# Kernel tuning notes

Hardware: AMD Instinct MI355X
Metric: run time of the kernel (lower is better)

The kernel has to match this reference:

```python
import jax, jax.numpy as jnp
import numpy as np

D_WIN = 6
SIGMA = D_WIN / 2.0  # sigma = D/2
EPS = 1e-6


def _ln(x, g, b):
    m = jnp.mean(x, -1, keepdims=True)
    v = jnp.var(x, -1, keepdims=True)
    return (x - m) / jnp.sqrt(v + EPS) * g + b


def _cross_attn(q, kv, Wq, Wkv, Wproj, bproj, nh):
    # standard multi-head cross attention, no qkv bias (qkv_bias=False)
    B, S, C = q.shape
    N = kv.shape[1]
    hd = C // nh
    scale = hd ** -0.5
    qh = (q @ Wq).reshape(B, S, nh, hd).transpose(0, 2, 1, 3) * scale
    kvh = (kv @ Wkv).reshape(B, N, 2, nh, hd).transpose(2, 0, 3, 1, 4)
    k, v = kvh[0], kvh[1]
    attn = jax.nn.softmax(jnp.einsum('bhsd,bhnd->bhsn', qh, k), -1)
    x = jnp.einsum('bhsn,bhnd->bhsd', attn, v).transpose(0, 2, 1, 3).reshape(B, S, C)
    return x @ Wproj + bproj


def setup_inputs() -> dict:
    key = jax.random.key(0)
    ks = jax.random.split(key, 32)
    B, S, C, H, W = 32, 128, 384, 8, 512

    def lin(k, i, o):
        return jax.random.normal(k, (i, o), jnp.float32) * 0.02

    inp = {
        'q': jax.random.normal(ks[0], (B, S, C), jnp.float32),
        'kv': jax.random.normal(ks[1], (B, H * W, C), jnp.float32),
        # main attention linears (qkv_bias=False)
        'Wq': lin(ks[2], C, C),
        'Wkv': lin(ks[3], C, 2 * C),
        'Wproj': lin(ks[4], C, C), 'bproj': jnp.zeros((C,), jnp.float32),
        # position predictor
        'Wp_w': lin(ks[5], C, C), 'Wp_b': jnp.zeros((C,), jnp.float32),
        'vp_w': lin(ks[6], C, 1), 'vp_b': jnp.zeros((1,), jnp.float32),
        'Wqpos': lin(ks[7], C, C), 'bqpos': jnp.zeros((C,), jnp.float32),
        # simplified RCTC decoder projection
        'Wrctc': lin(ks[8], C, C), 'brctc': jnp.zeros((C,), jnp.float32),
        # pt_to_question cross attention (2 heads)
        'ca1_Wq': lin(ks[9], C, C), 'ca1_Wkv': lin(ks[10], C, 2 * C),
        'ca1_Wproj': lin(ks[11], C, C), 'ca1_bproj': jnp.zeros((C,), jnp.float32),
        # pt_to_image cross attention (2 heads)
        'ca2_Wq': lin(ks[12], C, C), 'ca2_Wkv': lin(ks[13], C, 2 * C),
        'ca2_Wproj': lin(ks[14], C, C), 'ca2_bproj': jnp.zeros((C,), jnp.float32),
        # layernorms
        'g_q1': jnp.ones((C,), jnp.float32), 'b_q1': jnp.zeros((C,), jnp.float32),
        'g_kv1': jnp.ones((C,), jnp.float32), 'b_kv1': jnp.zeros((C,), jnp.float32),
        'g_q2': jnp.ones((C,), jnp.float32), 'b_q2': jnp.zeros((C,), jnp.float32),
        'g_kv2': jnp.ones((C,), jnp.float32), 'b_kv2': jnp.zeros((C,), jnp.float32),
        'sz_h': H, 'sz_w': W,
    }
    return inp


def reference(q, kv, Wq, Wkv, Wproj, bproj, Wp_w, Wp_b, vp_w, vp_b, Wqpos, bqpos,
              Wrctc, brctc, ca1_Wq, ca1_Wkv, ca1_Wproj, ca1_bproj,
              ca2_Wq, ca2_Wkv, ca2_Wproj, ca2_bproj,
              g_q1, b_q1, g_kv1, b_kv1, g_q2, b_q2, g_kv2, b_kv2, sz_h, sz_w):
    B, N, C = kv.shape
    S = q.shape[1]
    H, W = sz_h, sz_w
    nh = 1
    hd = C // nh
    scale = hd ** -0.5

    # RCTC decoder (simplified): (B,N,C) -> (B,C,H,W) -> collapse H -> (B,W,C) -> linear
    kv_img = kv.transpose(0, 2, 1).reshape(B, C, H, W)
    dec = kv_img.mean(axis=2).transpose(0, 2, 1)  # (B, W, C)
    dec = dec @ Wrctc + brctc

    qh = (q @ Wq).reshape(B, S, nh, hd).transpose(0, 2, 1, 3) * scale  # (B,nh,S,hd)
    kvh = (dec @ Wkv).reshape(B, W, 2, nh, hd).transpose(2, 0, 3, 1, 4)
    k, v = kvh[0], kvh[1]  # (B,nh,W,hd)

    # position prediction branch
    p = q @ Wqpos + bqpos
    p = _cross_attn(_ln(p, g_q1, b_q1), _ln(q, g_kv1, b_kv1),
                    ca1_Wq, ca1_Wkv, ca1_Wproj, ca1_bproj, 2)
    p = _cross_attn(_ln(p, g_q2, b_q2), _ln(dec, g_kv2, b_kv2),
                    ca2_Wq, ca2_Wkv, ca2_Wproj, ca2_bproj, 2)
    p_t = jax.nn.sigmoid(jnp.tanh(p @ Wp_w + Wp_b) @ vp_w + vp_b) * W  # (B,S,1)

    # Gaussian window mask around predicted position
    idx = jnp.arange(W, dtype=jnp.float32)[None, None, None, :]     # (1,1,1,W)
    pexp = p_t[:, None, :, :]                                        # (B,1,S,1)
    gauss = jnp.exp(-(idx - pexp) ** 2 / (2.0 * SIGMA ** 2))         # (B,1,S,W)

    attn = jnp.einsum('bhsd,bhwd->bhsw', qh, k) * gauss
    attn = jax.nn.softmax(attn, -1)
    x = jnp.einsum('bhsw,bhwd->bhsd', attn, v).transpose(0, 2, 1, 3).reshape(B, S, C)
    return x @ Wproj + bproj
```

## Files before the change

kernel.cpp:

```cpp
#include <hip/hip_runtime.h>
#include <hip/hip_bf16.h>
#include <math.h>

#define B_ 32
#define S_ 128
#define C_ 384
#define H_ 8
#define W_ 512
#define NKV 4096

typedef __attribute__((ext_vector_type(8))) short short8;
typedef __attribute__((ext_vector_type(4))) float floatx4;

static __device__ __forceinline__ ushort f2bf(float v) {
    __hip_bfloat16 h = __float2bfloat16(v);
    return *(ushort*)&h;
}
static __device__ __forceinline__ float ldf(const float* p, size_t i) { return p[i]; }
static __device__ __forceinline__ float ldf(const ushort* p, size_t i) {
    union { uint u; float f; } c; c.u = (uint)p[i] << 16; return c.f;
}

static __device__ __forceinline__ void gl_lds16(const ushort* g, ushort* l) {
    __builtin_amdgcn_global_load_lds(
        (const __attribute__((address_space(1))) void*)g,
        (__attribute__((address_space(3))) void*)l, 16, 0, 0);
}

__global__ __launch_bounds__(256) void mean_kernel(const float* __restrict__ kv,
                                                   ushort* __restrict__ dec0b) {
    int v = blockIdx.x * blockDim.x + threadIdx.x;
    int total = B_ * W_ * (C_ / 4);
    if (v >= total) return;
    int c4  = v % (C_ / 4);
    int row = v / (C_ / 4);
    int b = row / W_;
    int w = row % W_;
    const float4* src = (const float4*)kv + (size_t)(b * NKV + w) * (C_ / 4) + c4;
    float4 s = {0.f, 0.f, 0.f, 0.f};
#pragma unroll
    for (int h = 0; h < H_; ++h) {
        float4 t = src[(size_t)h * W_ * (C_ / 4)];
        s.x += t.x; s.y += t.y; s.z += t.z; s.w += t.w;
    }
    ushort4 o;
    o.x = f2bf(s.x * 0.125f); o.y = f2bf(s.y * 0.125f);
    o.z = f2bf(s.z * 0.125f); o.w = f2bf(s.w * 0.125f);
    ((ushort4*)dec0b)[v] = o;
}

__global__ __launch_bounds__(256) void cast_kernel(const float* __restrict__ in,
                                                   ushort* __restrict__ out, int n4) {
    int v = blockIdx.x * blockDim.x + threadIdx.x;
    if (v >= n4) return;
    float4 f = ((const float4*)in)[v];
    ushort4 o;
    o.x = f2bf(f.x); o.y = f2bf(f.y); o.z = f2bf(f.z); o.w = f2bf(f.w);
    ((ushort4*)out)[v] = o;
}

struct WtDesc { const float* src[12]; ushort* dst[12]; int Kd[12]; int Nd[12]; };
__global__ __launch_bounds__(256) void wtcast_kernel(WtDesc d) {
    int wi = blockIdx.y;
    int idx = blockIdx.x * 256 + threadIdx.x;
    int K = d.Kd[wi], N = d.Nd[wi];
    if (idx >= K * N) return;
    int n = idx / K, k = idx % K;
    d.dst[wi][idx] = f2bf(d.src[wi][(size_t)k * N + n]);
}

__global__ __launch_bounds__(256) void bgemm_kernel(
    const ushort* __restrict__ A, const ushort* __restrict__ Bt,
    const float* __restrict__ bias, float* __restrict__ Cout,
    ushort* __restrict__ Cbf, int M, int N, int K, float alpha, int act)
{
    __shared__ ushort As[128 * 32];
    __shared__ ushort Bs[128 * 32];
    const int tid = threadIdx.x;
    const int bm = blockIdx.y * 128, bn = blockIdx.x * 128;
    const int wav = tid >> 6, lane = tid & 63;
    const int wm = (wav >> 1) * 64, wn = (wav & 1) * 64;
    const int lrow = lane & 15, lq = lane >> 4;

    floatx4 acc[4][4] = {};

    const int crow = tid >> 2, ccol = (tid & 3) * 8;
    const ushort* Ag0 = A + (size_t)(bm + crow) * K + ccol;
    const ushort* Ag1 = Ag0 + (size_t)64 * K;
    const ushort* Bg0 = Bt + (size_t)(bn + crow) * K + ccol;
    const ushort* Bg1 = Bg0 + (size_t)64 * K;
    ushort* AsP0 = &As[tid * 8];
    ushort* AsP1 = &As[2048 + tid * 8];
    ushort* BsP0 = &Bs[tid * 8];
    ushort* BsP1 = &Bs[2048 + tid * 8];

    for (int k0 = 0; k0 < K; k0 += 32) {
        gl_lds16(Ag0 + k0, AsP0);
        gl_lds16(Ag1 + k0, AsP1);
        gl_lds16(Bg0 + k0, BsP0);
        gl_lds16(Bg1 + k0, BsP1);
        __syncthreads();
        short8 af[4], bfr[4];
#pragma unroll
        for (int i = 0; i < 4; ++i)
            af[i] = *(const short8*)&As[(wm + 16 * i + lrow) * 32 + lq * 8];
#pragma unroll
        for (int j = 0; j < 4; ++j)
            bfr[j] = *(const short8*)&Bs[(wn + 16 * j + lrow) * 32 + lq * 8];
#pragma unroll
        for (int i = 0; i < 4; ++i)
#pragma unroll
            for (int j = 0; j < 4; ++j)
                acc[i][j] = __builtin_amdgcn_mfma_f32_16x16x32_bf16(af[i], bfr[j], acc[i][j], 0, 0, 0);
        __syncthreads();
    }

#pragma unroll
    for (int i = 0; i < 4; ++i)
#pragma unroll
        for (int j = 0; j < 4; ++j) {
            int row = bm + wm + 16 * i + lq * 4;
            int col = bn + wn + 16 * j + lrow;
            float bv = bias ? bias[col] : 0.f;
#pragma unroll
            for (int r = 0; r < 4; ++r) {
                float v = acc[i][j][r] * alpha + bv;
                if (act == 1) v = tanhf(v);
                size_t off = (size_t)(row + r) * N + col;
                if (Cout) Cout[off] = v;
                if (Cbf) Cbf[off] = f2bf(v);
            }
        }
}

static inline void bgemm(hipStream_t st, const ushort* A, const ushort* Bt,
                         const float* bias, float* Cout, ushort* Cbf,
                         int M, int N, int K, float alpha, int act) {
    dim3 grid(N / 128, M / 128), block(256);
    bgemm_kernel<<<grid, block, 0, st>>>(A, Bt, bias, Cout, Cbf, M, N, K, alpha, act);
}

struct BGArgs {
    const ushort* A; const ushort* Bt;
    const float* bias; float* outF; ushort* outB;
    int lda, ldb, ldo;
    long AsB, BsB, OsB;
    int AsH, BsH, OsH;
    int K, NH;
    float alpha; int act;
};
__global__ __launch_bounds__(256) void battn_kernel(BGArgs g) {
    __shared__ ushort As[128 * 40];
    __shared__ ushort Bs[64 * 40];
    const int bn = blockIdx.x * 64, bm = blockIdx.y * 128;
    const int bat = blockIdx.z, bb = bat / g.NH, hh = bat % g.NH;
    const ushort* A  = g.A  + (size_t)bb * g.AsB + (size_t)hh * g.AsH;
    const ushort* Bt = g.Bt + (size_t)bb * g.BsB + (size_t)hh * g.BsH;
    const int tid = threadIdx.x;
    const int wav = tid >> 6, lane = tid & 63;
    const int lrow = lane & 15, lq = lane >> 4;
    const int sr = tid >> 2, sc0 = (tid & 3) * 8;
    const ushort* Ag0 = A + (size_t)(bm + sr) * g.lda + sc0;
    const ushort* Ag1 = A + (size_t)(bm + sr + 64) * g.lda + sc0;
    const ushort* Bg  = Bt + (size_t)(bn + sr) * g.ldb + sc0;
    ushort* Asw0 = &As[sr * 40 + sc0];
    ushort* Asw1 = &As[(sr + 64) * 40 + sc0];
    ushort* Bsw  = &Bs[sr * 40 + sc0];

    floatx4 acc[2][4] = {};

    for (int k0 = 0; k0 < g.K; k0 += 32) {
        uint4 a0 = *(const uint4*)(Ag0 + k0);
        uint4 a1 = *(const uint4*)(Ag1 + k0);
        uint4 b  = *(const uint4*)(Bg + k0);
        __syncthreads();
        *(uint4*)Asw0 = a0; *(uint4*)Asw1 = a1; *(uint4*)Bsw = b;
        __syncthreads();
        short8 af0 = *(const short8*)&As[(wav * 32 + lrow) * 40 + lq * 8];
        short8 af1 = *(const short8*)&As[(wav * 32 + 16 + lrow) * 40 + lq * 8];
#pragma unroll
        for (int j = 0; j < 4; ++j) {
            short8 bf = *(const short8*)&Bs[(16 * j + lrow) * 40 + lq * 8];
            acc[0][j] = __builtin_amdgcn_mfma_f32_16x16x32_bf16(af0, bf, acc[0][j], 0, 0, 0);
            acc[1][j] = __builtin_amdgcn_mfma_f32_16x16x32_bf16(af1, bf, acc[1][j], 0, 0, 0);
        }
    }

#pragma unroll
    for (int i = 0; i < 2; ++i)
#pragma unroll
        for (int j = 0; j < 4; ++j) {
            int col = bn + 16 * j + lrow;
            float bv = g.bias ? g.bias[col] : 0.f;
            int row0 = bm + wav * 32 + 16 * i + lq * 4;
#pragma unroll
            for (int r = 0; r < 4; ++r) {
                float v = acc[i][j][r] * g.alpha + bv;
                if (g.act == 1) v = tanhf(v);
                size_t off = (size_t)bb * g.OsB + (size_t)hh * g.OsH
                           + (size_t)(row0 + r) * g.ldo + col;
                if (g.outF) g.outF[off] = v;
                if (g.outB) g.outB[off] = f2bf(v);
            }
        }
}

static inline void battn(hipStream_t st, const ushort* A, const ushort* Bt,
                         const float* bias, float* outF, ushort* outB,
                         int M, int N, int K, float alpha, int act,
                         int lda, long AsB, int AsH,
                         int ldb, long BsB, int BsH,
                         int ldo, long OsB, int OsH,
                         int NH, int nbat) {
    BGArgs g;
    g.A = A; g.Bt = Bt; g.bias = bias; g.outF = outF; g.outB = outB;
    g.lda = lda; g.ldb = ldb; g.ldo = ldo;
    g.AsB = AsB; g.BsB = BsB; g.OsB = OsB;
    g.AsH = AsH; g.BsH = BsH; g.OsH = OsH;
    g.K = K; g.NH = NH; g.alpha = alpha; g.act = act;
    dim3 grid(N / 64, M / 128, nbat);
    battn_kernel<<<grid, 256, 0, st>>>(g);
}

static inline void bgemm64(hipStream_t st, const ushort* A, const ushort* Bt,
                           const float* bias, float* outF, ushort* outB,
                           int M, int N, int K, float alpha, int act) {
    battn(st, A, Bt, bias, outF, outB, M, N, K, alpha, act,
          K, 0, 0, K, 0, 0, N, 0, 0, 1, 1);
}

template <typename T>
__global__ __launch_bounds__(128) void ln_kernel(const T* __restrict__ X,
    const float* __restrict__ g, const float* __restrict__ bb,
    ushort* __restrict__ Y) {
    int row = blockIdx.x;
    const T* x = X + (size_t)row * C_;
    ushort* y = Y + (size_t)row * C_;
    int t = threadIdx.x;
    float v0 = ldf(x, t), v1 = ldf(x, t + 128), v2 = ldf(x, t + 256);
    float s = v0 + v1 + v2, sq = v0 * v0 + v1 * v1 + v2 * v2;
    __shared__ float rs[128], rq[128];
    rs[t] = s; rq[t] = sq; __syncthreads();
    if (t < 64) {
        s = rs[t] + rs[t + 64]; sq = rq[t] + rq[t + 64];
        for (int o = 32; o; o >>= 1) { s += __shfl_down(s, o); sq += __shfl_down(sq, o); }
        if (t == 0) { rs[0] = s; rq[0] = sq; }
    }
    __syncthreads();
    float mean = rs[0] * (1.0f / C_);
    float var  = rq[0] * (1.0f / C_) - mean * mean;
    float inv  = rsqrtf(var + 1e-6f);
    y[t]       = f2bf((v0 - mean) * inv * g[t]       + bb[t]);
    y[t + 128] = f2bf((v1 - mean) * inv * g[t + 128] + bb[t + 128]);
    y[t + 256] = f2bf((v2 - mean) * inv * g[t + 256] + bb[t + 256]);
}

template <int NW, int GAUSS>
__global__ __launch_bounds__(256) void softmax_kernel(
    const float* __restrict__ sc, const float* __restrict__ ptv,
    ushort* __restrict__ P)
{
    int row = blockIdx.x * 4 + (threadIdx.x >> 6);
    int lane = threadIdx.x & 63;
    const float* s = sc + (size_t)row * NW;
    float pcen = GAUSS ? ptv[row] : 0.f;
    float vals[NW / 64];
    float m = -1e30f;
#pragma unroll
    for (int i = 0; i < NW / 64; ++i) {
        int w = lane + 64 * i;
        float v = s[w];
        if (GAUSS) { float dw = (float)w - pcen; v *= expf(dw * dw * (-1.0f / 18.0f)); }
        vals[i] = v; m = fmaxf(m, v);
    }
#pragma unroll
    for (int o = 32; o; o >>= 1) m = fmaxf(m, __shfl_xor(m, o));
    float sum = 0.f;
#pragma unroll
    for (int i = 0; i < NW / 64; ++i) { vals[i] = expf(vals[i] - m); sum += vals[i]; }
#pragma unroll
    for (int o = 32; o; o >>= 1) sum += __shfl_xor(sum, o);
    float rinv = 1.0f / sum;
    ushort* op = P + (size_t)row * NW;
#pragma unroll
    for (int i = 0; i < NW / 64; ++i) op[lane + 64 * i] = f2bf(vals[i] * rinv);
}

__global__ __launch_bounds__(256) void vtrans_kernel(
    const ushort* __restrict__ kvb, ushort* __restrict__ vt,
    int Nw, int C2, int CC)
{
    int b = blockIdx.z;
    int w0 = blockIdx.x * 32, c0 = blockIdx.y * 32;
    __shared__ ushort t[32][33];
    int tid = threadIdx.x;
    int wl = tid >> 3, c4 = (tid & 7) * 4;
    ushort4 v = *(const ushort4*)&kvb[((size_t)b * Nw + w0 + wl) * C2 + CC + c0 + c4];
    t[wl][c4] = v.x; t[wl][c4 + 1] = v.y; t[wl][c4 + 2] = v.z; t[wl][c4 + 3] = v.w;
    __syncthreads();
    int dl = tid >> 3, w4 = (tid & 7) * 4;
    ushort4 o;
    o.x = t[w4][dl]; o.y = t[w4 + 1][dl]; o.z = t[w4 + 2][dl]; o.w = t[w4 + 3][dl];
    *(ushort4*)&vt[((size_t)b * CC + c0 + dl) * Nw + w0 + w4] = o;
}

__global__ __launch_bounds__(128) void pt_kernel(const float* __restrict__ T,
    const float* __restrict__ vpw, const float* __restrict__ vpb,
    float* __restrict__ out) {
    int row = blockIdx.x;
    int t = threadIdx.x;
    const float* x = T + (size_t)row * C_;
    float s = x[t] * vpw[t] + x[t + 128] * vpw[t + 128] + x[t + 256] * vpw[t + 256];
    __shared__ float red[128];
    red[t] = s; __syncthreads();
    if (t < 64) {
        s = red[t] + red[t + 64];
        for (int o = 32; o; o >>= 1) s += __shfl_down(s, o);
        if (t == 0) {
            float z = s + vpb[0];
            out[row] = 512.0f / (1.0f + expf(-z));
        }
    }
}

extern "C" void kernel_launch(void* const* d_in, const int* in_sizes, int n_in,
                              void* d_out, int out_size, void* d_ws, size_t ws_size,
                              hipStream_t stream) {
    const float* q     = (const float*)d_in[0];
    const float* kv    = (const float*)d_in[1];
    const float* Wq    = (const float*)d_in[2];
    const float* Wkv   = (const float*)d_in[3];
    const float* Wproj = (const float*)d_in[4];
    const float* bproj = (const float*)d_in[5];
    const float* Wp_w  = (const float*)d_in[6];
    const float* Wp_b  = (const float*)d_in[7];
    const float* vp_w  = (const float*)d_in[8];
    const float* vp_b  = (const float*)d_in[9];
    const float* Wqpos = (const float*)d_in[10];
    const float* bqpos = (const float*)d_in[11];
    const float* Wrctc = (const float*)d_in[12];
    const float* brctc = (const float*)d_in[13];
    const float* ca1_Wq    = (const float*)d_in[14];
    const float* ca1_Wkv   = (const float*)d_in[15];
    const float* ca1_Wproj = (const float*)d_in[16];
    const float* ca1_bproj = (const float*)d_in[17];
    const float* ca2_Wq    = (const float*)d_in[18];
    const float* ca2_Wkv   = (const float*)d_in[19];
    const float* ca2_Wproj = (const float*)d_in[20];
    const float* ca2_bproj = (const float*)d_in[21];
    const float* g_q1  = (const float*)d_in[22];
    const float* b_q1  = (const float*)d_in[23];
    const float* g_kv1 = (const float*)d_in[24];
    const float* b_kv1 = (const float*)d_in[25];
    const float* g_q2  = (const float*)d_in[26];
    const float* b_q2  = (const float*)d_in[27];
    const float* g_kv2 = (const float*)d_in[28];
    const float* b_kv2 = (const float*)d_in[29];
    float* out = (float*)d_out;
    float* ws  = (float*)d_ws;

    ushort* dec0b = (ushort*)(ws);
    ushort* wb    = (ushort*)(ws + 3145728);
    ushort* qb    = (ushort*)(ws + 4251648);
    ushort* decb  = (ushort*)(ws + 5038080);
    ushort* qhb   = (ushort*)(ws + 8183808);
    float*  p     = ws + 8970240;
    ushort* pb    = (ushort*)(ws + 10543104);
    float*  t1    = ws + 11329536;
    ushort* t1b   = (ushort*)(ws + 12902400);
    ushort* t2b   = (ushort*)(ws + 13688832);
    ushort* qpb   = (ushort*)(ws + 16834560);
    ushort* kvb   = (ushort*)(ws + 17620992);
    ushort* vt    = (ushort*)(ws + 23912448);
    float*  sc    = ws + 27058176;
    ushort* Pb    = (ushort*)(ws + 31252480);
    ushort* xb    = (ushort*)(ws + 33349632);
    float*  ptb   = ws + 34136064;

    ushort* wbWq     = wb;
    ushort* wbWqpos  = wb + 147456;
    ushort* wbWrctc  = wb + 294912;
    ushort* wbC1Wq   = wb + 442368;
    ushort* wbC1Wp   = wb + 589824;
    ushort* wbC2Wq   = wb + 737280;
    ushort* wbC2Wp   = wb + 884736;
    ushort* wbWpw    = wb + 1032192;
    ushort* wbWproj  = wb + 1179648;
    ushort* wbWkv    = wb + 1327104;
    ushort* wbC1Wkv  = wb + 1622016;
    ushort* wbC2Wkv  = wb + 1916928;

    const float rs384 = 0.05103103630798288f;
    const float rs192 = 0.07216878364870323f;

    mean_kernel<<<(B_ * W_ * (C_ / 4) + 255) / 256, 256, 0, stream>>>(kv, dec0b);
    {
        WtDesc d;
        const float* s_[12] = {Wq, Wqpos, Wrctc, ca1_Wq, ca1_Wproj, ca2_Wq, ca2_Wproj,
                               Wp_w, Wproj, Wkv, ca1_Wkv, ca2_Wkv};
        ushort* t_[12] = {wbWq, wbWqpos, wbWrctc, wbC1Wq, wbC1Wp, wbC2Wq, wbC2Wp,
                          wbWpw, wbWproj, wbWkv, wbC1Wkv, wbC2Wkv};
        for (int i = 0; i < 12; ++i) {
            d.src[i] = s_[i]; d.dst[i] = t_[i];
            d.Kd[i] = 384; d.Nd[i] = (i >= 9) ? 768 : 384;
        }
        dim3 grid((294912 + 255) / 256, 12);
        wtcast_kernel<<<grid, 256, 0, stream>>>(d);
        cast_kernel<<<(393216 + 255) / 256, 256, 0, stream>>>(q, qb, 393216);
    }
    bgemm(stream, dec0b, wbWrctc, brctc, nullptr, decb, B_ * W_, 384, 384, 1.f, 0);
    bgemm64(stream, qb, wbWq, nullptr, nullptr, qhb, B_ * S_, 384, 384, rs384, 0);
    bgemm64(stream, qb, wbWqpos, bqpos, p, nullptr, B_ * S_, 384, 384, 1.f, 0);
    ln_kernel<float><<<B_ * S_, 128, 0, stream>>>(p, g_q1, b_q1, t1b);
    ln_kernel<float><<<B_ * S_, 128, 0, stream>>>(q, g_kv1, b_kv1, t2b);
    bgemm64(stream, t1b, wbC1Wq, nullptr, nullptr, qpb, B_ * S_, 384, 384, rs192, 0);
    bgemm64(stream, t2b, wbC1Wkv, nullptr, nullptr, kvb, B_ * S_, 768, 384, 1.f, 0);
    {
        dim3 gt(S_ / 32, C_ / 32, B_);
        vtrans_kernel<<<gt, 256, 0, stream>>>(kvb, vt, S_, 768, 384);
    }
    battn(stream, qpb, kvb, nullptr, sc, nullptr, 128, 128, 192, 1.f, 0,
          384, (long)S_ * 384, 192,
          768, (long)S_ * 768, 192,
          128, (long)2 * S_ * 128, S_ * 128, 2, 64);
    softmax_kernel<128, 0><<<(B_ * 2 * S_) / 4, 256, 0, stream>>>(sc, nullptr, Pb);
    battn(stream, Pb, vt, nullptr, nullptr, xb, 128, 192, 128, 1.f, 0,
          128, (long)2 * S_ * 128, S_ * 128,
          128, (long)C_ * S_, 192 * S_,
          384, (long)S_ * 384, 192, 2, 64);
    bgemm64(stream, xb, wbC1Wp, ca1_bproj, p, nullptr, B_ * S_, 384, 384, 1.f, 0);
    ln_kernel<float><<<B_ * S_, 128, 0, stream>>>(p, g_q2, b_q2, t1b);
    ln_kernel<ushort><<<B_ * W_, 128, 0, stream>>>(decb, g_kv2, b_kv2, t2b);
    bgemm64(stream, t1b, wbC2Wq, nullptr, nullptr, qpb, B_ * S_, 384, 384, rs192, 0);
    bgemm(stream, t2b, wbC2Wkv, nullptr, nullptr, kvb, B_ * W_, 768, 384, 1.f, 0);
    {
        dim3 gt(W_ / 32, C_ / 32, B_);
        vtrans_kernel<<<gt, 256, 0, stream>>>(kvb, vt, W_, 768, 384);
    }
    battn(stream, qpb, kvb, nullptr, sc, nullptr, 128, 512, 192, 1.f, 0,
          384, (long)S_ * 384, 192,
          768, (long)W_ * 768, 192,
          512, (long)2 * S_ * 512, S_ * 512, 2, 64);
    softmax_kernel<512, 0><<<(B_ * 2 * S_) / 4, 256, 0, stream>>>(sc, nullptr, Pb);
    battn(stream, Pb, vt, nullptr, nullptr, xb, 128, 192, 512, 1.f, 0,
          512, (long)2 * S_ * 512, S_ * 512,
          512, (long)C_ * W_, 192 * W_,
          384, (long)S_ * 384, 192, 2, 64);
    bgemm64(stream, xb, wbC2Wp, ca2_bproj, p, pb, B_ * S_, 384, 384, 1.f, 0);
    bgemm64(stream, pb, wbWpw, Wp_b, t1, nullptr, B_ * S_, 384, 384, 1.f, 1);
    pt_kernel<<<B_ * S_, 128, 0, stream>>>(t1, vp_w, vp_b, ptb);
    bgemm(stream, decb, wbWkv, nullptr, nullptr, kvb, B_ * W_, 768, 384, 1.f, 0);
    {
        dim3 gt(W_ / 32, C_ / 32, B_);
        vtrans_kernel<<<gt, 256, 0, stream>>>(kvb, vt, W_, 768, 384);
    }
    battn(stream, qhb, kvb, nullptr, sc, nullptr, 128, 512, 384, 1.f, 0,
          384, (long)S_ * 384, 0,
          768, (long)W_ * 768, 0,
          512, (long)S_ * 512, 0, 1, 32);
    softmax_kernel<512, 1><<<(B_ * S_) / 4, 256, 0, stream>>>(sc, ptb, Pb);
    battn(stream, Pb, vt, nullptr, nullptr, xb, 128, 384, 512, 1.f, 0,
          512, (long)S_ * 512, 0,
          512, (long)C_ * W_, 0,
          384, (long)S_ * 384, 0, 1, 32);
    bgemm64(stream, xb, wbWproj, bproj, out, nullptr, B_ * S_, 384, 384, 1.f, 0);
}
```

Baseline: 639.8 us.

## Fuse QK^T scores with softmax into single attention kernel, merge layernorms, tile weight cast

Replaces the separate score GEMM plus softmax pair with one kernel per attention. It computes QK^T with MFMA into registers, applies the optional Gaussian window, runs the softmax with cross-wave reductions in LDS, and writes bf16 probabilities directly. This removes the fp32 score matrix round-trip through global memory and several launches. The paired layernorm launches are merged into a single kernel, and the weight transpose-cast now goes through an LDS tile so reads and writes are coalesced. In exchange the fused kernel holds many accumulators and uses a lot of LDS for the large head-dim case, which may limit occupancy.

```diff
diff --git a/kernel.cpp b/kernel.cpp
--- a/kernel.cpp
+++ b/kernel.cpp
@@ -62,11 +62,22 @@
 struct WtDesc { const float* src[12]; ushort* dst[12]; int Kd[12]; int Nd[12]; };
 __global__ __launch_bounds__(256) void wtcast_kernel(WtDesc d) {
     int wi = blockIdx.y;
-    int idx = blockIdx.x * 256 + threadIdx.x;
     int K = d.Kd[wi], N = d.Nd[wi];
-    if (idx >= K * N) return;
-    int n = idx / K, k = idx % K;
-    d.dst[wi][idx] = f2bf(d.src[wi][(size_t)k * N + n]);
+    int tiles_n = N / 32;
+    int tile = blockIdx.x;
+    if (tile >= (K / 32) * tiles_n) return;
+    int k0 = (tile / tiles_n) * 32, n0 = (tile % tiles_n) * 32;
+    __shared__ float t[32][33];
+    int tid = threadIdx.x;
+    int r = tid >> 3, c4 = (tid & 7) * 4;
+    float4 v = *(const float4*)&d.src[wi][(size_t)(k0 + r) * N + n0 + c4];
+    t[r][c4] = v.x; t[r][c4 + 1] = v.y; t[r][c4 + 2] = v.z; t[r][c4 + 3] = v.w;
+    __syncthreads();
+    int c = tid >> 3, k4 = (tid & 7) * 4;
+    ushort4 o;
+    o.x = f2bf(t[k4][c]); o.y = f2bf(t[k4 + 1][c]);
+    o.z = f2bf(t[k4 + 2][c]); o.w = f2bf(t[k4 + 3][c]);
+    *(ushort4*)&d.dst[wi][(size_t)(n0 + c) * K + k0 + k4] = o;
 }
 
 __global__ __launch_bounds__(256) void bgemm_kernel(
@@ -229,15 +240,163 @@
           K, 0, 0, K, 0, 0, N, 0, 0, 1, 1);
 }
 
-template <typename T>
-__global__ __launch_bounds__(128) void ln_kernel(const T* __restrict__ X,
-    const float* __restrict__ g, const float* __restrict__ bb,
-    ushort* __restrict__ Y) {
+template <int NW, int HD, int MT, int GAUSS, int NH>
+__global__ __launch_bounds__(256) void attn_sm_kernel(
+    const ushort* __restrict__ Q, const ushort* __restrict__ Kt,
+    const float* __restrict__ ptv, ushort* __restrict__ P)
+{
+    constexpr int NC = NW / 64, MF = MT / 16, KS = HD / 32;
+    constexpr int HDP = HD + 8, NWP = NW + 8;
+    __shared__ ushort Qs[MT * HDP];
+    __shared__ ushort Ks[64 * HDP];
+    __shared__ ushort Ps[MT * NWP];
+    __shared__ float redm[4][MT];
+    __shared__ float reds[4][MT];
+    __shared__ float pts[MT];
+
+    const int tid = threadIdx.x;
+    const int wav = tid >> 6, lane = tid & 63;
+    const int lrow = lane & 15, lq = lane >> 4;
+    const int z = blockIdx.z, b = z / NH, hh = z % NH;
+    const int mt0 = blockIdx.x * MT;
+
+    const ushort* Qg = Q + ((size_t)b * S_ + mt0) * C_ + hh * HD;
+    for (int i = tid; i < MT * (HD / 8); i += 256) {
+        int m = i / (HD / 8), c8 = (i % (HD / 8)) * 8;
+        *(uint4*)&Qs[m * HDP + c8] = *(const uint4*)&Qg[(size_t)m * C_ + c8];
+    }
+    if (GAUSS && tid < MT) pts[tid] = ptv[(size_t)z * S_ + mt0 + tid];
+    __syncthreads();
+
+    short8 qreg[KS][MF];
+#pragma unroll
+    for (int ks = 0; ks < KS; ++ks)
+#pragma unroll
+        for (int mi = 0; mi < MF; ++mi)
+            qreg[ks][mi] = *(const short8*)&Qs[(16 * mi + lrow) * HDP + ks * 32 + lq * 8];
+
+    floatx4 acc[NC][MF] = {};
+    const ushort* Kg = Kt + (size_t)b * NW * 768 + hh * HD;
+    for (int c = 0; c < NC; ++c) {
+        __syncthreads();
+        for (int i = tid; i < 64 * (HD / 8); i += 256) {
+            int n = i / (HD / 8), c8 = (i % (HD / 8)) * 8;
+            *(uint4*)&Ks[n * HDP + c8] = *(const uint4*)&Kg[(size_t)(64 * c + n) * 768 + c8];
+        }
+        __syncthreads();
+#pragma unroll
+        for (int ks = 0; ks < KS; ++ks) {
+            short8 kf = *(const short8*)&Ks[(16 * wav + lrow) * HDP + ks * 32 + lq * 8];
+#pragma unroll
+            for (int mi = 0; mi < MF; ++mi)
+                acc[c][mi] = __builtin_amdgcn_mfma_f32_16x16x32_bf16(qreg[ks][mi], kf, acc[c][mi], 0, 0, 0);
+        }
+    }
+
+    float pl[MF][4];
+    if (GAUSS) {
+#pragma unroll
+        for (int mi = 0; mi < MF; ++mi)
+#pragma unroll
+            for (int r = 0; r < 4; ++r) pl[mi][r] = pts[16 * mi + lq * 4 + r];
+    }
+    float mrow[MF][4];
+#pragma unroll
+    for (int mi = 0; mi < MF; ++mi)
+#pragma unroll
+        for (int r = 0; r < 4; ++r) mrow[mi][r] = -1e30f;
+#pragma unroll
+    for (int c = 0; c < NC; ++c)
+#pragma unroll
+        for (int mi = 0; mi < MF; ++mi)
+#pragma unroll
+            for (int r = 0; r < 4; ++r) {
+                float v = acc[c][mi][r];
+                if (GAUSS) {
+                    float dw = (float)(64 * c + 16 * wav + lrow) - pl[mi][r];
+                    v *= expf(dw * dw * (-1.0f / 18.0f));
+                    acc[c][mi][r] = v;
+                }
+                mrow[mi][r] = fmaxf(mrow[mi][r], v);
+            }
+#pragma unroll
+    for (int o = 1; o < 16; o <<= 1)
+#pragma unroll
+        for (int mi = 0; mi < MF; ++mi)
+#pragma unroll
+            for (int r = 0; r < 4; ++r)
+                mrow[mi][r] = fmaxf(mrow[mi][r], __shfl_xor(mrow[mi][r], o));
+    if (lrow == 0)
+#pragma unroll
+        for (int mi = 0; mi < MF; ++mi)
+#pragma unroll
+            for (int r = 0; r < 4; ++r) redm[wav][16 * mi + lq * 4 + r] = mrow[mi][r];
+    __syncthreads();
+#pragma unroll
+    for (int mi = 0; mi < MF; ++mi)
+#pragma unroll
+        for (int r = 0; r < 4; ++r) {
+            int m = 16 * mi + lq * 4 + r;
+            mrow[mi][r] = fmaxf(fmaxf(redm[0][m], redm[1][m]), fmaxf(redm[2][m], redm[3][m]));
+        }
+    float srow[MF][4] = {};
+#pragma unroll
+    for (int c = 0; c < NC; ++c)
+#pragma unroll
+        for (int mi = 0; mi < MF; ++mi)
+#pragma unroll
+            for (int r = 0; r < 4; ++r) {
+                float e = expf(acc[c][mi][r] - mrow[mi][r]);
+                acc[c][mi][r] = e;
+                srow[mi][r] += e;
+            }
+#pragma unroll
+    for (int o = 1; o < 16; o <<= 1)
+#pragma unroll
+        for (int mi = 0; mi < MF; ++mi)
+#pragma unroll
+            for (int r = 0; r < 4; ++r) srow[mi][r] += __shfl_xor(srow[mi][r], o);
+    if (lrow == 0)
+#pragma unroll
+        for (int mi = 0; mi < MF; ++mi)
+#pragma unroll
+            for (int r = 0; r < 4; ++r) reds[wav][16 * mi + lq * 4 + r] = srow[mi][r];
+    __syncthreads();
+#pragma unroll
+    for (int mi = 0; mi < MF; ++mi)
+#pragma unroll
+        for (int r = 0; r < 4; ++r) {
+            int m = 16 * mi + lq * 4 + r;
+            float s = reds[0][m] + reds[1][m] + reds[2][m] + reds[3][m];
+            float rinv = 1.0f / s;
+#pragma unroll
+            for (int c = 0; c < NC; ++c)
+                Ps[m * NWP + 64 * c + 16 * wav + lrow] = f2bf(acc[c][mi][r] * rinv);
+        }
+    __syncthreads();
+    ushort* Pg = P + ((size_t)z * S_ + mt0) * NW;
+    for (int i = tid; i < MT * (NW / 8); i += 256) {
+        int m = i / (NW / 8), c8 = (i % (NW / 8)) * 8;
+        *(uint4*)&Pg[(size_t)m * NW + c8] = *(const uint4*)&Ps[m * NWP + c8];
+    }
+}
+
+struct Ln2Desc {
+    const void* X0; const float* g0; const float* b0; ushort* Y0; int bf0; int rows0;
+    const void* X1; const float* g1; const float* b1; ushort* Y1; int bf1;
+};
+__global__ __launch_bounds__(128) void ln2_kernel(Ln2Desc d) {
     int row = blockIdx.x;
-    const T* x = X + (size_t)row * C_;
+    const void* X; const float* g; const float* bb; ushort* Y; int isbf;
+    if (row < d.rows0) { X = d.X0; g = d.g0; bb = d.b0; Y = d.Y0; isbf = d.bf0; }
+    else { row -= d.rows0; X = d.X1; g = d.g1; bb = d.b1; Y = d.Y1; isbf = d.bf1; }
+    const float*  xf = (const float*)X + (size_t)row * C_;
+    const ushort* xb = (const ushort*)X + (size_t)row * C_;
     ushort* y = Y + (size_t)row * C_;
     int t = threadIdx.x;
-    float v0 = ldf(x, t), v1 = ldf(x, t + 128), v2 = ldf(x, t + 256);
+    float v0, v1, v2;
+    if (isbf) { v0 = ldf(xb, t); v1 = ldf(xb, t + 128); v2 = ldf(xb, t + 256); }
+    else      { v0 = ldf(xf, t); v1 = ldf(xf, t + 128); v2 = ldf(xf, t + 256); }
     float s = v0 + v1 + v2, sq = v0 * v0 + v1 * v1 + v2 * v2;
     __shared__ float rs[128], rq[128];
     rs[t] = s; rq[t] = sq; __syncthreads();
@@ -253,37 +412,6 @@
     y[t]       = f2bf((v0 - mean) * inv * g[t]       + bb[t]);
     y[t + 128] = f2bf((v1 - mean) * inv * g[t + 128] + bb[t + 128]);
     y[t + 256] = f2bf((v2 - mean) * inv * g[t + 256] + bb[t + 256]);
-}
-
-template <int NW, int GAUSS>
-__global__ __launch_bounds__(256) void softmax_kernel(
-    const float* __restrict__ sc, const float* __restrict__ ptv,
-    ushort* __restrict__ P)
-{
-    int row = blockIdx.x * 4 + (threadIdx.x >> 6);
-    int lane = threadIdx.x & 63;
-    const float* s = sc + (size_t)row * NW;
-    float pcen = GAUSS ? ptv[row] : 0.f;
-    float vals[NW / 64];
-    float m = -1e30f;
-#pragma unroll
-    for (int i = 0; i < NW / 64; ++i) {
-        int w = lane + 64 * i;
-        float v = s[w];
-        if (GAUSS) { float dw = (float)w - pcen; v *= expf(dw * dw * (-1.0f / 18.0f)); }
-        vals[i] = v; m = fmaxf(m, v);
-    }
-#pragma unroll
-    for (int o = 32; o; o >>= 1) m = fmaxf(m, __shfl_xor(m, o));
-    float sum = 0.f;
-#pragma unroll
-    for (int i = 0; i < NW / 64; ++i) { vals[i] = expf(vals[i] - m); sum += vals[i]; }
-#pragma unroll
-    for (int o = 32; o; o >>= 1) sum += __shfl_xor(sum, o);
-    float rinv = 1.0f / sum;
-    ushort* op = P + (size_t)row * NW;
-#pragma unroll
-    for (int i = 0; i < NW / 64; ++i) op[lane + 64 * i] = f2bf(vals[i] * rinv);
 }
 
 __global__ __launch_bounds__(256) void vtrans_kernel(
@@ -372,7 +500,6 @@
     ushort* qpb   = (ushort*)(ws + 16834560);
     ushort* kvb   = (ushort*)(ws + 17620992);
     ushort* vt    = (ushort*)(ws + 23912448);
-    float*  sc    = ws + 27058176;
     ushort* Pb    = (ushort*)(ws + 31252480);
     ushort* xb    = (ushort*)(ws + 33349632);
     float*  ptb   = ws + 34136064;
@@ -404,44 +531,46 @@
             d.src[i] = s_[i]; d.dst[i] = t_[i];
             d.Kd[i] = 384; d.Nd[i] = (i >= 9) ? 768 : 384;
         }
-        dim3 grid((294912 + 255) / 256, 12);
+        dim3 grid(288, 12);
         wtcast_kernel<<<grid, 256, 0, stream>>>(d);
         cast_kernel<<<(393216 + 255) / 256, 256, 0, stream>>>(q, qb, 393216);
     }
     bgemm(stream, dec0b, wbWrctc, brctc, nullptr, decb, B_ * W_, 384, 384, 1.f, 0);
     bgemm64(stream, qb, wbWq, nullptr, nullptr, qhb, B_ * S_, 384, 384, rs384, 0);
     bgemm64(stream, qb, wbWqpos, bqpos, p, nullptr, B_ * S_, 384, 384, 1.f, 0);
-    ln_kernel<float><<<B_ * S_, 128, 0, stream>>>(p, g_q1, b_q1, t1b);
-    ln_kernel<float><<<B_ * S_, 128, 0, stream>>>(q, g_kv1, b_kv1, t2b);
+    {
+        Ln2Desc d;
+        d.X0 = p; d.g0 = g_q1;  d.b0 = b_q1;  d.Y0 = t1b; d.bf0 = 0; d.rows0 = B_ * S_;
+        d.X1 = q; d.g1 = g_kv1; d.b1 = b_kv1; d.Y1 = t2b; d.bf1 = 0;
+        ln2_kernel<<<2 * B_ * S_, 128, 0, stream>>>(d);
+    }
     bgemm64(stream, t1b, wbC1Wq, nullptr, nullptr, qpb, B_ * S_, 384, 384, rs192, 0);
     bgemm64(stream, t2b, wbC1Wkv, nullptr, nullptr, kvb, B_ * S_, 768, 384, 1.f, 0);
     {
         dim3 gt(S_ / 32, C_ / 32, B_);
         vtrans_kernel<<<gt, 256, 0, stream>>>(kvb, vt, S_, 768, 384);
     }
-    battn(stream, qpb, kvb, nullptr, sc, nullptr, 128, 128, 192, 1.f, 0,
-          384, (long)S_ * 384, 192,
-          768, (long)S_ * 768, 192,
-          128, (long)2 * S_ * 128, S_ * 128, 2, 64);
-    softmax_kernel<128, 0><<<(B_ * 2 * S_) / 4, 256, 0, stream>>>(sc, nullptr, Pb);
+    attn_sm_kernel<128, 192, 32, 0, 2><<<dim3(S_ / 32, 1, B_ * 2), 256, 0, stream>>>(
+        qpb, kvb, nullptr, Pb);
     battn(stream, Pb, vt, nullptr, nullptr, xb, 128, 192, 128, 1.f, 0,
           128, (long)2 * S_ * 128, S_ * 128,
           128, (long)C_ * S_, 192 * S_,
           384, (long)S_ * 384, 192, 2, 64);
     bgemm64(stream, xb, wbC1Wp, ca1_bproj, p, nullptr, B_ * S_, 384, 384, 1.f, 0);
-    ln_kernel<float><<<B_ * S_, 128, 0, stream>>>(p, g_q2, b_q2, t1b);
-    ln_kernel<ushort><<<B_ * W_, 128, 0, stream>>>(decb, g_kv2, b_kv2, t2b);
+    {
+        Ln2Desc d;
+        d.X0 = p;    d.g0 = g_q2;  d.b0 = b_q2;  d.Y0 = t1b; d.bf0 = 0; d.rows0 = B_ * S_;
+        d.X1 = decb; d.g1 = g_kv2; d.b1 = b_kv2; d.Y1 = t2b; d.bf1 = 1;
+        ln2_kernel<<<B_ * S_ + B_ * W_, 128, 0, stream>>>(d);
+    }
     bgemm64(stream, t1b, wbC2Wq, nullptr, nullptr, qpb, B_ * S_, 384, 384, rs192, 0);
     bgemm(stream, t2b, wbC2Wkv, nullptr, nullptr, kvb, B_ * W_, 768, 384, 1.f, 0);
     {
         dim3 gt(W_ / 32, C_ / 32, B_);
         vtrans_kernel<<<gt, 256, 0, stream>>>(kvb, vt, W_, 768, 384);
     }
-    battn(stream, qpb, kvb, nullptr, sc, nullptr, 128, 512, 192, 1.f, 0,
-          384, (long)S_ * 384, 192,
-          768, (long)W_ * 768, 192,
-          512, (long)2 * S_ * 512, S_ * 512, 2, 64);
-    softmax_kernel<512, 0><<<(B_ * 2 * S_) / 4, 256, 0, stream>>>(sc, nullptr, Pb);
+    attn_sm_kernel<512, 192, 32, 0, 2><<<dim3(S_ / 32, 1, B_ * 2), 256, 0, stream>>>(
+        qpb, kvb, nullptr, Pb);
     battn(stream, Pb, vt, nullptr, nullptr, xb, 128, 192, 512, 1.f, 0,
           512, (long)2 * S_ * 512, S_ * 512,
           512, (long)C_ * W_, 192 * W_,
@@ -454,11 +583,8 @@
         dim3 gt(W_ / 32, C_ / 32, B_);
         vtrans_kernel<<<gt, 256, 0, stream>>>(kvb, vt, W_, 768, 384);
     }
-    battn(stream, qhb, kvb, nullptr, sc, nullptr, 128, 512, 384, 1.f, 0,
-          384, (long)S_ * 384, 0,
-          768, (long)W_ * 768, 0,
-          512, (long)S_ * 512, 0, 1, 32);
-    softmax_kernel<512, 1><<<(B_ * S_) / 4, 256, 0, stream>>>(sc, ptb, Pb);
+    attn_sm_kernel<512, 384, 16, 1, 1><<<dim3(S_ / 16, 1, B_), 256, 0, stream>>>(
+        qhb, kvb, ptb, Pb);
     battn(stream, Pb, vt, nullptr, nullptr, xb, 128, 384, 512, 1.f, 0,
           512, (long)S_ * 512, 0,
           512, (long)C_ * W_, 0,
```

New measurement: 663.3 us. +3.7%, slower.
